# Optimization experiments

Hardware: AMD Instinct MI355X
Metric: run time of the kernel (lower is better)

## Reference

```python
import jax, jax.numpy as jnp
import numpy as np

D_MODEL = 1024
NHEAD = 16
HEAD_DIM = D_MODEL // NHEAD
LN_EPS = 1e-5


def _retention_scan(v, lam_h):
    # v: (B, L, H, DH); lam_h: (H,)
    # recurrence: s_0 = v_0; s_t = lam * s_{t-1} + v_t
    B, L, H, DH = v.shape
    a = jnp.broadcast_to(lam_h[None, None, :, None], v.shape)

    def combine(x, y):
        a1, b1 = x
        a2, b2 = y
        return (a1 * a2, a2 * b1 + b2)

    _, states = jax.lax.associative_scan(combine, (a, v), axis=1)
    return states


def setup_inputs() -> dict:
    key = jax.random.key(0)
    ks = jax.random.split(key, 6)
    B, L, D = 4, 4096, D_MODEL
    s = 1.0 / np.sqrt(D)
    return {
        "x": jax.random.normal(ks[0], (B, L, D), jnp.float32),
        "Wq": jax.random.normal(ks[1], (D, D), jnp.float32) * s,
        "Wv": jax.random.normal(ks[2], (D, D), jnp.float32) * s,
        "Wg": jax.random.normal(ks[3], (D, D), jnp.float32) * s,
        "Wo": jax.random.normal(ks[4], (D, D), jnp.float32) * s,
        "beta": jnp.full((NHEAD,), -0.2, jnp.float32),
        "ln_gamma": jnp.ones((D_MODEL,), jnp.float32),
        "ln_beta": jnp.zeros((D_MODEL,), jnp.float32),
    }


def reference(x, Wq, Wv, Wg, Wo, beta, ln_gamma, ln_beta):
    B, L, D = x.shape
    H, DH = NHEAD, HEAD_DIM
    # projections (torch Linear: x @ W.T)
    q = (x @ Wq.T).reshape(B, L, H, DH)
    v = (x @ Wv.T).reshape(B, L, H, DH)
    lam_h = jax.nn.sigmoid(beta)
    state = _retention_scan(v, lam_h)  # (B, L, H, DH)
    y = (q * state).reshape(B, L, D)
    # LayerNorm over last dim
    mu = jnp.mean(y, axis=-1, keepdims=True)
    var = jnp.mean((y - mu) ** 2, axis=-1, keepdims=True)
    y = (y - mu) * jax.lax.rsqrt(var + LN_EPS) * ln_gamma + ln_beta
    # SiLU gate
    gate = jax.nn.silu(x @ Wg.T)
    y = y * gate
    return y @ Wo.T
```

## Files before the change

### kernel.cpp

```cpp
#include <hip/hip_runtime.h>

#define BB 4
#define LL 4096
#define DM 1024
#define NH 16
#define MM (BB * LL)
#define CC2 256
#define LC2 16

#define BKT 64
#define NKT (DM / BKT)

typedef unsigned short u16;
typedef float f32x4 __attribute__((ext_vector_type(4)));
typedef int i32x4 __attribute__((ext_vector_type(4)));
typedef __bf16 mfma_in __attribute__((ext_vector_type(8)));

__device__ __forceinline__ u16 f2bf(float f) {
    unsigned u = __float_as_uint(f);
    u += 0x7FFFu + ((u >> 16) & 1u);
    return (u16)(u >> 16);
}
__device__ __forceinline__ float bf2f(u16 u) {
    return __uint_as_float(((unsigned)u) << 16);
}

__device__ __forceinline__ void gld_lds16(const u16* g, u16* l) {
    __builtin_amdgcn_global_load_lds(
        (const __attribute__((address_space(1))) void*)g,
        (__attribute__((address_space(3))) void*)l,
        16, 0, 0);
}

__device__ __forceinline__ mfma_in ds_read128(const u16* p) {
    i32x4 r;
    unsigned off = (unsigned)(size_t)(const __attribute__((address_space(3))) u16*)p;
    asm volatile("ds_read_b128 %0, %1" : "=v"(r) : "v"(off));
    return __builtin_bit_cast(mfma_in, r);
}

#define XF4 (MM * DM / 4)
#define WF4 (DM * DM / 4)
__global__ __launch_bounds__(256)
void cvt_all(const float* __restrict__ x,
             const float* __restrict__ w0, const float* __restrict__ w1,
             const float* __restrict__ w2, const float* __restrict__ w3,
             u16* __restrict__ dst) {
    int i = blockIdx.x * 256 + threadIdx.x;
    const float* src;
    int si;
    if (i < XF4) { src = x; si = i; }
    else {
        int j = i - XF4;
        const float* ws[4] = {w0, w1, w2, w3};
        src = ws[j >> 18];
        si = j & (WF4 - 1);
    }
    float4 f = ((const float4*)src)[si];
    ushort4 o;
    o.x = f2bf(f.x); o.y = f2bf(f.y); o.z = f2bf(f.z); o.w = f2bf(f.w);
    ((ushort4*)dst)[i] = o;
}


template<int IOFF, int JOFF>
__device__ __forceinline__ void mfmaQ(const mfma_in (&a)[4][2], const mfma_in (&b)[2][2],
                                      f32x4 (&acc)[8][4]) {
#pragma unroll
    for (int s = 0; s < 2; s++)
#pragma unroll
        for (int i = 0; i < 4; i++)
#pragma unroll
            for (int j = 0; j < 2; j++)
                acc[IOFF + i][JOFF + j] = __builtin_amdgcn_mfma_f32_16x16x32_bf16(
                    a[i][s], b[j][s], acc[IOFF + i][JOFF + j], 0, 0, 0);
}

#define PH_MID() do { \
    __builtin_amdgcn_s_barrier(); \
    asm volatile("s_waitcnt lgkmcnt(0)"); \
    __builtin_amdgcn_sched_barrier(0); \
    __builtin_amdgcn_s_setprio(1); \
} while (0)

#define PH_END() do { \
    __builtin_amdgcn_s_setprio(0); \
    __builtin_amdgcn_sched_barrier(0); \
    __builtin_amdgcn_s_barrier(); \
} while (0)

#define PH_END_VM() do { \
    __builtin_amdgcn_s_setprio(0); \
    __builtin_amdgcn_sched_barrier(0); \
    asm volatile("s_waitcnt vmcnt(4)"); \
    __builtin_amdgcn_s_barrier(); \
} while (0)

__device__ __forceinline__ void mainloop256(
    const u16* __restrict__ A, const u16* __restrict__ B,
    int mBlk, int nBlk,
    u16 (*__restrict__ As)[256 * 64], u16 (*__restrict__ Bs)[256 * 64],
    f32x4 (&acc)[8][4]) {
    const int tid  = threadIdx.x;
    const int wave = tid >> 6;
    const int lane = tid & 63;
    const int quad = lane >> 4;
    const int l16  = lane & 15;
    const int wm   = (wave >> 2) * 128;
    const int wn   = (wave & 3) * 64;

    const int sRow = wave * 8 + (lane >> 3);
    const int sCol = ((lane & 7) ^ (lane >> 3)) * 8;
    const u16* gA = A + (size_t)(mBlk + sRow) * DM + sCol;
    const u16* gB = B + (size_t)(nBlk + sRow) * DM + sCol;
    const int ldsW = wave * 8 * 64;

    int rA[8], rB[4];
#pragma unroll
    for (int i = 0; i < 8; i++) rA[i] = (wm + i * 16 + l16) * 64;
#pragma unroll
    for (int j = 0; j < 4; j++) rB[j] = (wn + j * 16 + l16) * 64;
    const int c0 = ((quad    ) ^ (l16 & 7)) * 8;
    const int c1 = ((quad + 4) ^ (l16 & 7)) * 8;

#define STG_A(buf, h, t) do { \
    const int kk_ = ((t) & (NKT - 1)) * BKT; \
    gld_lds16(gA + (size_t)((h) * 128) * DM + kk_,      &As[buf][((h) * 128) * 64 + ldsW]); \
    gld_lds16(gA + (size_t)((h) * 128 + 64) * DM + kk_, &As[buf][((h) * 128 + 64) * 64 + ldsW]); \
} while (0)
#define STG_B(buf, h, t) do { \
    const int kk_ = ((t) & (NKT - 1)) * BKT; \
    gld_lds16(gB + (size_t)((h) * 128) * DM + kk_,      &Bs[buf][((h) * 128) * 64 + ldsW]); \
    gld_lds16(gB + (size_t)((h) * 128 + 64) * DM + kk_, &Bs[buf][((h) * 128 + 64) * 64 + ldsW]); \
} while (0)
#define LDA(dst, buf, i, s) (dst) = ds_read128(&As[buf][rA[i] + ((s) ? c1 : c0)])
#define LDB(dst, buf, j, s) (dst) = ds_read128(&Bs[buf][rB[j] + ((s) ? c1 : c0)])

    mfma_in aL[4][2], aH[4][2], bL[2][2], bH[2][2];

    STG_A(0, 0, 0); STG_A(0, 1, 0);
    STG_B(0, 0, 0); STG_B(0, 1, 0);
    STG_A(1, 0, 1); STG_A(1, 1, 1);
    asm volatile("s_waitcnt vmcnt(4)");
    __builtin_amdgcn_s_barrier();

#pragma unroll 1
    for (int it = 0; it < NKT / 2; ++it) {
        const int k = 2 * it;

#pragma unroll
        for (int i = 0; i < 4; i++) { LDA(aL[i][0], 0, i, 0); LDA(aL[i][1], 0, i, 1); }
#pragma unroll
        for (int j = 0; j < 2; j++) { LDB(bL[j][0], 0, j, 0); LDB(bL[j][1], 0, j, 1); }
        STG_B(1, 0, k + 1);
        PH_MID();
        mfmaQ<0, 0>(aL, bL, acc);
        PH_END();

#pragma unroll
        for (int i = 0; i < 4; i++) { LDA(aH[i][0], 0, i + 4, 0); LDA(aH[i][1], 0, i + 4, 1); }
        STG_B(1, 1, k + 1);
        PH_MID();
        mfmaQ<4, 0>(aH, bL, acc);
        PH_END();

#pragma unroll
        for (int j = 0; j < 2; j++) { LDB(bH[j][0], 0, j + 2, 0); LDB(bH[j][1], 0, j + 2, 1); }
        STG_A(0, 0, k + 2);
        PH_MID();
        mfmaQ<0, 2>(aL, bH, acc);
        PH_END();

        STG_A(0, 1, k + 2);
        PH_MID();
        mfmaQ<4, 2>(aH, bH, acc);
        PH_END_VM();

#pragma unroll
        for (int i = 0; i < 4; i++) { LDA(aL[i][0], 1, i, 0); LDA(aL[i][1], 1, i, 1); }
#pragma unroll
        for (int j = 0; j < 2; j++) { LDB(bL[j][0], 1, j, 0); LDB(bL[j][1], 1, j, 1); }
        STG_B(0, 0, k + 2);
        PH_MID();
        mfmaQ<0, 0>(aL, bL, acc);
        PH_END();

#pragma unroll
        for (int i = 0; i < 4; i++) { LDA(aH[i][0], 1, i + 4, 0); LDA(aH[i][1], 1, i + 4, 1); }
        STG_B(0, 1, k + 2);
        PH_MID();
        mfmaQ<4, 0>(aH, bL, acc);
        PH_END();

#pragma unroll
        for (int j = 0; j < 2; j++) { LDB(bH[j][0], 1, j + 2, 0); LDB(bH[j][1], 1, j + 2, 1); }
        STG_A(1, 0, k + 3);
        PH_MID();
        mfmaQ<0, 2>(aL, bH, acc);
        PH_END();

        STG_A(1, 1, k + 3);
        PH_MID();
        mfmaQ<4, 2>(aH, bH, acc);
        PH_END_VM();
    }
#undef STG_A
#undef STG_B
#undef LDA
#undef LDB
}

__global__ __launch_bounds__(512, 2)
void gemm_qvg(const u16* __restrict__ A, const u16* __restrict__ B,
              u16* __restrict__ oq, u16* __restrict__ ov, u16* __restrict__ og) {
    __shared__ __align__(16) u16 As[2][256 * 64];
    __shared__ __align__(16) u16 Bs[2][256 * 64];
    const int mBlk = blockIdx.x * 256;
    const int nBlk = blockIdx.y * 256;

    f32x4 acc[8][4] = {};
    mainloop256(A, B, mBlk, nBlk, As, Bs, acc);

    const int tid  = threadIdx.x;
    const int wave = tid >> 6;
    const int lane = tid & 63;
    const int quad = lane >> 4;
    const int l16  = lane & 15;
    const int wm   = (wave >> 2) * 128;
    const int wn   = (wave & 3) * 64;

    u16* outs[3] = {oq, ov, og};
    u16* O = outs[nBlk >> 10];
    const int nIn = nBlk & 1023;
#pragma unroll
    for (int i = 0; i < 8; i++) {
        int row0 = mBlk + wm + i * 16 + quad * 4;
#pragma unroll
        for (int j = 0; j < 4; j++) {
            int col = nIn + wn + j * 16 + l16;
#pragma unroll
            for (int r = 0; r < 4; r++)
                O[(size_t)(row0 + r) * DM + col] = f2bf(acc[i][j][r]);
        }
    }
}

__global__ __launch_bounds__(512, 2)
void gemm_out(const u16* __restrict__ A, const u16* __restrict__ B,
              float* __restrict__ C) {
    __shared__ __align__(16) u16 As[2][256 * 64];
    __shared__ __align__(16) u16 Bs[2][256 * 64];
    const int mBlk = blockIdx.x * 256;
    const int nBlk = blockIdx.y * 256;

    f32x4 acc[8][4] = {};
    mainloop256(A, B, mBlk, nBlk, As, Bs, acc);

    const int tid  = threadIdx.x;
    const int wave = tid >> 6;
    const int lane = tid & 63;
    const int quad = lane >> 4;
    const int l16  = lane & 15;
    const int wm   = (wave >> 2) * 128;
    const int wn   = (wave & 3) * 64;

#pragma unroll
    for (int i = 0; i < 8; i++) {
        int row0 = mBlk + wm + i * 16 + quad * 4;
#pragma unroll
        for (int j = 0; j < 4; j++) {
            int col = nBlk + wn + j * 16 + l16;
#pragma unroll
            for (int r = 0; r < 4; r++)
                C[(size_t)(row0 + r) * DM + col] = acc[i][j][r];
        }
    }
}

__global__ __launch_bounds__(256)
void scan_ends(const u16* __restrict__ v, const float* __restrict__ beta,
               float* __restrict__ ebuf) {
    int d = blockIdx.x * 256 + threadIdx.x;
    int c = blockIdx.y, b = blockIdx.z;
    int h = d >> 6;
    float lam = 1.0f / (1.0f + __expf(-beta[h]));
    size_t idx = ((size_t)b * LL + (size_t)c * LC2) * DM + d;
    float s = 0.0f;
#pragma unroll
    for (int i = 0; i < LC2; i++) {
        s = lam * s + bf2f(v[idx]);
        idx += DM;
    }
    ebuf[((size_t)b * CC2 + c) * DM + d] = s;
}

__global__ __launch_bounds__(256)
void scan_carry(const float* __restrict__ ebuf, const float* __restrict__ beta,
                float* __restrict__ carry) {
    int ch = blockIdx.x * 256 + threadIdx.x;
    int b = ch >> 10, d = ch & 1023;
    int h = d >> 6;
    float lam = 1.0f / (1.0f + __expf(-beta[h]));
    float lamC = lam;
    for (int i = 0; i < 4; i++) lamC *= lamC;
    float cur = 0.0f;
#pragma unroll 8
    for (int c = 0; c < CC2; c++) {
        size_t idx = ((size_t)b * CC2 + c) * DM + d;
        carry[idx] = cur;
        cur = lamC * cur + ebuf[idx];
    }
}

__global__ __launch_bounds__(256)
void scan_ln_gate(const u16* __restrict__ v, const u16* __restrict__ q,
                  const u16* __restrict__ g, const float* __restrict__ carry,
                  const float* __restrict__ beta, const float* __restrict__ gamma,
                  const float* __restrict__ lnb, u16* __restrict__ out) {
    __shared__ float red[2][8];
    const int t = threadIdx.x;
    const int c = blockIdx.x, b = blockIdx.y;
    const int wave = t >> 6, lane = t & 63;
    const int d0 = t * 4;
    const int h = d0 >> 6;
    float lam = 1.0f / (1.0f + __expf(-beta[h]));
    float4 gm = ((const float4*)gamma)[t];
    float4 bt = ((const float4*)lnb)[t];
    float4 cr = *(const float4*)(carry + ((size_t)b * CC2 + c) * DM + d0);
    float s0 = cr.x, s1 = cr.y, s2 = cr.z, s3 = cr.w;
    size_t base = ((size_t)b * LL + (size_t)c * LC2) * DM + d0;

    for (int i = 0; i < LC2; i++) {
        ushort4 v4 = *(const ushort4*)(v + base);
        ushort4 q4 = *(const ushort4*)(q + base);
        ushort4 g4 = *(const ushort4*)(g + base);
        s0 = lam * s0 + bf2f(v4.x);
        s1 = lam * s1 + bf2f(v4.y);
        s2 = lam * s2 + bf2f(v4.z);
        s3 = lam * s3 + bf2f(v4.w);
        float y0 = bf2f(q4.x) * s0, y1 = bf2f(q4.y) * s1;
        float y2 = bf2f(q4.z) * s2, y3 = bf2f(q4.w) * s3;
        float sum = y0 + y1 + y2 + y3;
        float sq  = y0 * y0 + y1 * y1 + y2 * y2 + y3 * y3;
#pragma unroll
        for (int off = 32; off > 0; off >>= 1) {
            sum += __shfl_xor(sum, off);
            sq  += __shfl_xor(sq, off);
        }
        int p = i & 1;
        if (lane == 0) { red[p][wave] = sum; red[p][4 + wave] = sq; }
        __syncthreads();
        float ts = red[p][0] + red[p][1] + red[p][2] + red[p][3];
        float tq = red[p][4] + red[p][5] + red[p][6] + red[p][7];
        float mu  = ts * (1.0f / DM);
        float inv = rsqrtf(tq * (1.0f / DM) - mu * mu + 1e-5f);

        float gv0 = bf2f(g4.x), gv1 = bf2f(g4.y), gv2 = bf2f(g4.z), gv3 = bf2f(g4.w);
        float x0 = ((y0 - mu) * inv * gm.x + bt.x) * (gv0 / (1.0f + __expf(-gv0)));
        float x1 = ((y1 - mu) * inv * gm.y + bt.y) * (gv1 / (1.0f + __expf(-gv1)));
        float x2 = ((y2 - mu) * inv * gm.z + bt.z) * (gv2 / (1.0f + __expf(-gv2)));
        float x3 = ((y3 - mu) * inv * gm.w + bt.w) * (gv3 / (1.0f + __expf(-gv3)));
        ushort4 o;
        o.x = f2bf(x0); o.y = f2bf(x1); o.z = f2bf(x2); o.w = f2bf(x3);
        *(ushort4*)(out + base) = o;
        base += DM;
    }
}

extern "C" void kernel_launch(void* const* d_in, const int* in_sizes, int n_in,
                              void* d_out, int out_size, void* d_ws, size_t ws_size,
                              hipStream_t stream) {
    const float* x     = (const float*)d_in[0];
    const float* Wq    = (const float*)d_in[1];
    const float* Wv    = (const float*)d_in[2];
    const float* Wg    = (const float*)d_in[3];
    const float* Wo    = (const float*)d_in[4];
    const float* beta  = (const float*)d_in[5];
    const float* gamma = (const float*)d_in[6];
    const float* lnb   = (const float*)d_in[7];

    u16* xb  = (u16*)d_ws;
    u16* Wqb = xb + (size_t)MM * DM;
    u16* Wob = Wqb + (size_t)3 * DM * DM;
    u16* qb  = Wob + (size_t)DM * DM;
    u16* vb  = qb + (size_t)MM * DM;
    u16* gb  = vb + (size_t)MM * DM;
    float* ebuf  = (float*)(gb + (size_t)MM * DM);
    float* carry = ebuf + (size_t)BB * CC2 * DM;
    u16* yfin = xb;

    cvt_all<<<(XF4 + 4 * WF4 + 255) / 256, 256, 0, stream>>>(x, Wq, Wv, Wg, Wo, xb);

    dim3 gq(MM / 256, 3 * DM / 256);
    gemm_qvg<<<gq, 512, 0, stream>>>(xb, Wqb, qb, vb, gb);

    dim3 gs(DM / 256, CC2, BB);
    scan_ends<<<gs, 256, 0, stream>>>(vb, beta, ebuf);
    scan_carry<<<(BB * DM) / 256, 256, 0, stream>>>(ebuf, beta, carry);
    dim3 gf(CC2, BB);
    scan_ln_gate<<<gf, 256, 0, stream>>>(vb, qb, gb, carry, beta, gamma, lnb, yfin);

    dim3 go(MM / 256, DM / 256);
    gemm_out<<<go, 512, 0, stream>>>(yfin, Wob, (float*)d_out);
}
```

Measured before the change: 316.3 us.

## Restructure GEMM mainloop into per-k-tile double buffer with one barrier

Replaces the 8-phase ping-pong schedule, which put two block barriers around every MFMA quarter, with a simpler loop over k-tiles. Each iteration issues the next tile's global-to-LDS loads and overlaps fine-grained LDS reads, split by k half, with MFMA groups using lgkmcnt waits, then ends with one vmcnt(0) and one barrier. The aim is to cut barrier overhead and let waves drift so memory and compute interleave. The cost is that waiting for all global loads at the end of every tile may expose load latency, since only one tile is prefetched ahead.

```diff
diff --git a/kernel.cpp b/kernel.cpp
--- a/kernel.cpp
+++ b/kernel.cpp
@@ -64,36 +64,19 @@
 
 
 template<int IOFF, int JOFF>
-__device__ __forceinline__ void mfmaQ(const mfma_in (&a)[4][2], const mfma_in (&b)[2][2],
+__device__ __forceinline__ void mfma8(const mfma_in (&a)[4], const mfma_in (&b)[2],
                                       f32x4 (&acc)[8][4]) {
 #pragma unroll
-    for (int s = 0; s < 2; s++)
-#pragma unroll
-        for (int i = 0; i < 4; i++)
-#pragma unroll
-            for (int j = 0; j < 2; j++)
-                acc[IOFF + i][JOFF + j] = __builtin_amdgcn_mfma_f32_16x16x32_bf16(
-                    a[i][s], b[j][s], acc[IOFF + i][JOFF + j], 0, 0, 0);
-}
-
-#define PH_MID() do { \
-    __builtin_amdgcn_s_barrier(); \
-    asm volatile("s_waitcnt lgkmcnt(0)"); \
+    for (int i = 0; i < 4; i++)
+#pragma unroll
+        for (int j = 0; j < 2; j++)
+            acc[IOFF + i][JOFF + j] = __builtin_amdgcn_mfma_f32_16x16x32_bf16(
+                a[i], b[j], acc[IOFF + i][JOFF + j], 0, 0, 0);
+}
+
+#define WAITL(n) do { \
+    asm volatile("s_waitcnt lgkmcnt(" #n ")"); \
     __builtin_amdgcn_sched_barrier(0); \
-    __builtin_amdgcn_s_setprio(1); \
-} while (0)
-
-#define PH_END() do { \
-    __builtin_amdgcn_s_setprio(0); \
-    __builtin_amdgcn_sched_barrier(0); \
-    __builtin_amdgcn_s_barrier(); \
-} while (0)
-
-#define PH_END_VM() do { \
-    __builtin_amdgcn_s_setprio(0); \
-    __builtin_amdgcn_sched_barrier(0); \
-    asm volatile("s_waitcnt vmcnt(4)"); \
-    __builtin_amdgcn_s_barrier(); \
 } while (0)
 
 __device__ __forceinline__ void mainloop256(
@@ -123,91 +106,100 @@
     const int c0 = ((quad    ) ^ (l16 & 7)) * 8;
     const int c1 = ((quad + 4) ^ (l16 & 7)) * 8;
 
-#define STG_A(buf, h, t) do { \
+#define STG4_A(dst, t) do { \
     const int kk_ = ((t) & (NKT - 1)) * BKT; \
-    gld_lds16(gA + (size_t)((h) * 128) * DM + kk_,      &As[buf][((h) * 128) * 64 + ldsW]); \
-    gld_lds16(gA + (size_t)((h) * 128 + 64) * DM + kk_, &As[buf][((h) * 128 + 64) * 64 + ldsW]); \
+    gld_lds16(gA + kk_,                   (dst) + ldsW); \
+    gld_lds16(gA + (size_t) 64 * DM + kk_, (dst) +  64 * 64 + ldsW); \
+    gld_lds16(gA + (size_t)128 * DM + kk_, (dst) + 128 * 64 + ldsW); \
+    gld_lds16(gA + (size_t)192 * DM + kk_, (dst) + 192 * 64 + ldsW); \
 } while (0)
-#define STG_B(buf, h, t) do { \
+#define STG4_B(dst, t) do { \
     const int kk_ = ((t) & (NKT - 1)) * BKT; \
-    gld_lds16(gB + (size_t)((h) * 128) * DM + kk_,      &Bs[buf][((h) * 128) * 64 + ldsW]); \
-    gld_lds16(gB + (size_t)((h) * 128 + 64) * DM + kk_, &Bs[buf][((h) * 128 + 64) * 64 + ldsW]); \
+    gld_lds16(gB + kk_,                   (dst) + ldsW); \
+    gld_lds16(gB + (size_t) 64 * DM + kk_, (dst) +  64 * 64 + ldsW); \
+    gld_lds16(gB + (size_t)128 * DM + kk_, (dst) + 128 * 64 + ldsW); \
+    gld_lds16(gB + (size_t)192 * DM + kk_, (dst) + 192 * 64 + ldsW); \
 } while (0)
-#define LDA(dst, buf, i, s) (dst) = ds_read128(&As[buf][rA[i] + ((s) ? c1 : c0)])
-#define LDB(dst, buf, j, s) (dst) = ds_read128(&Bs[buf][rB[j] + ((s) ? c1 : c0)])
-
-    mfma_in aL[4][2], aH[4][2], bL[2][2], bH[2][2];
-
-    STG_A(0, 0, 0); STG_A(0, 1, 0);
-    STG_B(0, 0, 0); STG_B(0, 1, 0);
-    STG_A(1, 0, 1); STG_A(1, 1, 1);
-    asm volatile("s_waitcnt vmcnt(4)");
+#define RDA(dst, idx, cc) (dst) = ds_read128(curA + rA[idx] + (cc))
+#define RDB(dst, idx, cc) (dst) = ds_read128(curB + rB[idx] + (cc))
+
+    mfma_in aLs0[4], aHs0[4], bLs0[2], bHs0[2];
+    mfma_in aLs1[4], aHs1[4], bLs1[2], bHs1[2];
+
+    STG4_A(As[0], 0);
+    STG4_B(Bs[0], 0);
+    asm volatile("s_waitcnt vmcnt(0)");
     __builtin_amdgcn_s_barrier();
 
 #pragma unroll 1
-    for (int it = 0; it < NKT / 2; ++it) {
-        const int k = 2 * it;
-
-#pragma unroll
-        for (int i = 0; i < 4; i++) { LDA(aL[i][0], 0, i, 0); LDA(aL[i][1], 0, i, 1); }
-#pragma unroll
-        for (int j = 0; j < 2; j++) { LDB(bL[j][0], 0, j, 0); LDB(bL[j][1], 0, j, 1); }
-        STG_B(1, 0, k + 1);
-        PH_MID();
-        mfmaQ<0, 0>(aL, bL, acc);
-        PH_END();
-
-#pragma unroll
-        for (int i = 0; i < 4; i++) { LDA(aH[i][0], 0, i + 4, 0); LDA(aH[i][1], 0, i + 4, 1); }
-        STG_B(1, 1, k + 1);
-        PH_MID();
-        mfmaQ<4, 0>(aH, bL, acc);
-        PH_END();
-
-#pragma unroll
-        for (int j = 0; j < 2; j++) { LDB(bH[j][0], 0, j + 2, 0); LDB(bH[j][1], 0, j + 2, 1); }
-        STG_A(0, 0, k + 2);
-        PH_MID();
-        mfmaQ<0, 2>(aL, bH, acc);
-        PH_END();
-
-        STG_A(0, 1, k + 2);
-        PH_MID();
-        mfmaQ<4, 2>(aH, bH, acc);
-        PH_END_VM();
-
-#pragma unroll
-        for (int i = 0; i < 4; i++) { LDA(aL[i][0], 1, i, 0); LDA(aL[i][1], 1, i, 1); }
-#pragma unroll
-        for (int j = 0; j < 2; j++) { LDB(bL[j][0], 1, j, 0); LDB(bL[j][1], 1, j, 1); }
-        STG_B(0, 0, k + 2);
-        PH_MID();
-        mfmaQ<0, 0>(aL, bL, acc);
-        PH_END();
-
-#pragma unroll
-        for (int i = 0; i < 4; i++) { LDA(aH[i][0], 1, i + 4, 0); LDA(aH[i][1], 1, i + 4, 1); }
-        STG_B(0, 1, k + 2);
-        PH_MID();
-        mfmaQ<4, 0>(aH, bL, acc);
-        PH_END();
-
-#pragma unroll
-        for (int j = 0; j < 2; j++) { LDB(bH[j][0], 1, j + 2, 0); LDB(bH[j][1], 1, j + 2, 1); }
-        STG_A(1, 0, k + 3);
-        PH_MID();
-        mfmaQ<0, 2>(aL, bH, acc);
-        PH_END();
-
-        STG_A(1, 1, k + 3);
-        PH_MID();
-        mfmaQ<4, 2>(aH, bH, acc);
-        PH_END_VM();
-    }
-#undef STG_A
-#undef STG_B
-#undef LDA
-#undef LDB
+    for (int kt = 0; kt < NKT; ++kt) {
+        const int cur = kt & 1, nxt = cur ^ 1;
+        const u16* curA = As[cur];
+        const u16* curB = Bs[cur];
+
+#pragma unroll
+        for (int i = 0; i < 4; i++) RDA(aLs0[i], i, c0);
+#pragma unroll
+        for (int j = 0; j < 2; j++) RDB(bLs0[j], j, c0);
+#pragma unroll
+        for (int i = 0; i < 4; i++) RDA(aHs0[i], i + 4, c0);
+        STG4_A(As[nxt], kt + 1);
+        __builtin_amdgcn_sched_barrier(0);
+
+        WAITL(4);
+        __builtin_amdgcn_s_setprio(1);
+        mfma8<0, 0>(aLs0, bLs0, acc);
+        __builtin_amdgcn_s_setprio(0);
+
+#pragma unroll
+        for (int j = 0; j < 2; j++) RDB(bHs0[j], j + 2, c0);
+        WAITL(2);
+        __builtin_amdgcn_s_setprio(1);
+        mfma8<4, 0>(aHs0, bLs0, acc);
+        __builtin_amdgcn_s_setprio(0);
+
+#pragma unroll
+        for (int i = 0; i < 4; i++) RDA(aLs1[i], i, c1);
+        WAITL(4);
+        __builtin_amdgcn_s_setprio(1);
+        mfma8<0, 2>(aLs0, bHs0, acc);
+        mfma8<4, 2>(aHs0, bHs0, acc);
+        __builtin_amdgcn_s_setprio(0);
+
+#pragma unroll
+        for (int j = 0; j < 2; j++) RDB(bLs1[j], j, c1);
+#pragma unroll
+        for (int i = 0; i < 4; i++) RDA(aHs1[i], i + 4, c1);
+        STG4_B(Bs[nxt], kt + 1);
+        __builtin_amdgcn_sched_barrier(0);
+
+        WAITL(4);
+        __builtin_amdgcn_s_setprio(1);
+        mfma8<0, 0>(aLs1, bLs1, acc);
+        __builtin_amdgcn_s_setprio(0);
+
+#pragma unroll
+        for (int j = 0; j < 2; j++) RDB(bHs1[j], j + 2, c1);
+        WAITL(2);
+        __builtin_amdgcn_s_setprio(1);
+        mfma8<4, 0>(aHs1, bLs1, acc);
+        __builtin_amdgcn_s_setprio(0);
+
+        WAITL(0);
+        __builtin_amdgcn_s_setprio(1);
+        mfma8<0, 2>(aLs1, bHs1, acc);
+        mfma8<4, 2>(aHs1, bHs1, acc);
+        __builtin_amdgcn_s_setprio(0);
+
+        __builtin_amdgcn_sched_barrier(0);
+        asm volatile("s_waitcnt vmcnt(0)");
+        __builtin_amdgcn_sched_barrier(0);
+        __builtin_amdgcn_s_barrier();
+    }
+#undef STG4_A
+#undef STG4_B
+#undef RDA
+#undef RDB
 }
 
 __global__ __launch_bounds__(512, 2)
```

After: 317.0 us. About the same (+0.2%).
